# Optimization experiments

Measured on AMD Instinct MI355X. Metric: run time of the kernel, lower is better.

Reference implementation:

```python
import jax, jax.numpy as jnp
import numpy as np
from jax import lax

MAX_SCALE = 4
SCALES = [2 ** i for i in range(1, MAX_SCALE + 1)]  # [2, 4, 8, 16]
EPS = 1e-6
BN_EPS = 1e-3  # keras BatchNormalization default epsilon


def _box_sum(x, r):
    # DepthwiseConv2D with ones kernel, SAME zero padding == box sum window
    return lax.reduce_window(x, 0.0, lax.add, (1, r, r, 1), (1, 1, 1, 1), 'SAME')


def setup_inputs() -> dict:
    key = jax.random.key(0)
    k1, k2 = jax.random.split(key)
    B, H, W, C, K = 4, 224, 224, 64, 8
    return {
        'x': jax.random.normal(k1, (B, H, W, C), dtype=jnp.float32),
        'ols_weights': jnp.ones((MAX_SCALE,), jnp.float32),
        'anchors': jax.random.normal(k2, (C, K), dtype=jnp.float32),
        'hist_widths': jnp.ones((C, K), jnp.float32),
        'bn_gamma': jnp.ones((C,), jnp.float32),
        'bn_beta': jnp.zeros((C,), jnp.float32),
        'bn_mean': jnp.zeros((C,), jnp.float32),
        'bn_var': jnp.ones((C,), jnp.float32),
    }


def reference(x, ols_weights, anchors, hist_widths, bn_gamma, bn_beta, bn_mean, bn_var):
    # --- sample min-max scaling to [0, 1] per sample ---
    xmin = jnp.min(x, axis=(1, 2, 3), keepdims=True)
    xmax = jnp.max(x, axis=(1, 2, 3), keepdims=True)
    xs = (x - xmin) / (xmax - xmin + EPS)

    # --- multi-scale box measures: [B,H,W,C,S] ---
    measures = jnp.stack([_box_sum(xs, r) for r in SCALES], axis=-1)

    # --- weighted OLS slope of log(measure) vs log(scale) -> local alpha ---
    ly = jnp.log(measures + EPS)                         # [B,H,W,C,S]
    lr = jnp.log(jnp.asarray(SCALES, jnp.float32))       # [S]
    w = ols_weights                                       # [S]
    wsum = jnp.sum(w)
    lr_bar = jnp.sum(w * lr) / wsum
    ly_bar = jnp.sum(w * ly, axis=-1, keepdims=True) / wsum
    dx = lr - lr_bar                                      # [S]
    num = jnp.sum(w * dx * (ly - ly_bar), axis=-1)        # [B,H,W,C]
    den = jnp.sum(w * dx * dx)
    alphas = num / den

    # --- batch norm (inference mode, training=False) ---
    a = bn_gamma * (alphas - bn_mean) * lax.rsqrt(bn_var + BN_EPS) + bn_beta

    # --- triangular soft histogram over k anchors, relu'd and summed ---
    hist = 1.0 - hist_widths * jnp.abs(a[..., None] - anchors)  # [B,H,W,C,K]
    soft_counts = jnp.sum(jax.nn.relu(hist), axis=-1)           # [B,H,W,C]

    return x + jax.nn.sigmoid(soft_counts)
```

## Files before the change

### kernel.cpp

```cpp
#include <hip/hip_runtime.h>
#include <math.h>

#define B 4
#define H 224
#define W 224
#define C 64
#define K 8
#define WC (W*C)
#define HWC (H*W*C)

__device__ inline float wave_reduce_min(float v) {
  #pragma unroll
  for (int off = 32; off > 0; off >>= 1)
    v = fminf(v, __shfl_down(v, off, 64));
  return v;
}
__device__ inline float wave_reduce_max(float v) {
  #pragma unroll
  for (int off = 32; off > 0; off >>= 1)
    v = fmaxf(v, __shfl_down(v, off, 64));
  return v;
}

__global__ __launch_bounds__(256) void k_minmax_part(const float* __restrict__ x,
                                                     float* __restrict__ scratch) {
  int s   = blockIdx.x >> 9;
  int blk = blockIdx.x & 511;
  const float4* xs = (const float4*)(x + (size_t)s * HWC);
  const int n4 = HWC / 4;
  float vmin = INFINITY, vmax = -INFINITY;
  for (int i = blk*256 + threadIdx.x; i < n4; i += 512*256) {
    float4 v = xs[i];
    vmin = fminf(vmin, fminf(fminf(v.x, v.y), fminf(v.z, v.w)));
    vmax = fmaxf(vmax, fmaxf(fmaxf(v.x, v.y), fmaxf(v.z, v.w)));
  }
  __shared__ float smin[4], smax[4];
  float wmin = wave_reduce_min(vmin), wmax = wave_reduce_max(vmax);
  int wave = threadIdx.x >> 6, lane = threadIdx.x & 63;
  if (lane == 0) { smin[wave] = wmin; smax[wave] = wmax; }
  __syncthreads();
  if (threadIdx.x == 0) {
    float m = fminf(fminf(smin[0], smin[1]), fminf(smin[2], smin[3]));
    float M = fmaxf(fmaxf(smax[0], smax[1]), fmaxf(smax[2], smax[3]));
    scratch[blockIdx.x]        = m;
    scratch[2048 + blockIdx.x] = M;
  }
}

__global__ __launch_bounds__(256) void k_vpfx4(const float* __restrict__ x,
                                               const float* __restrict__ scratch,
                                               float* __restrict__ P) {
  int bid = blockIdx.x;
  int b = bid / W, w = bid % W;
  int seg = threadIdx.x >> 4;
  int chg = threadIdx.x & 15;
  int wv  = threadIdx.x >> 6;

  float vmn = fminf(scratch[b*512 + threadIdx.x], scratch[b*512 + 256 + threadIdx.x]);
  float vmx = fmaxf(scratch[2048 + b*512 + threadIdx.x], scratch[2048 + b*512 + 256 + threadIdx.x]);
  __shared__ float smin[4], smax[4];
  float wmn = wave_reduce_min(vmn), wmx = wave_reduce_max(vmx);
  if ((threadIdx.x & 63) == 0) { smin[wv] = wmn; smax[wv] = wmx; }
  __syncthreads();
  float xmin = fminf(fminf(smin[0], smin[1]), fminf(smin[2], smin[3]));
  float xmax = fmaxf(fmaxf(smax[0], smax[1]), fmaxf(smax[2], smax[3]));
  float inv  = 1.0f / (xmax - xmin + 1e-6f);

  const size_t colbase = (size_t)b*HWC + (size_t)w*C;
  const float4* xp4 = (const float4*)(x + colbase);
  const int RS4 = WC / 4;
  const int r0 = seg * 14;

  float4 v4[14];
  #pragma unroll
  for (int j = 0; j < 14; ++j) v4[j] = xp4[(size_t)(r0 + j) * RS4 + chg];

  float4 s4 = v4[0];
  #pragma unroll
  for (int j = 1; j < 14; ++j) {
    s4.x += v4[j].x; s4.y += v4[j].y; s4.z += v4[j].z; s4.w += v4[j].w;
  }

  __shared__ float4 segsum[16][16];
  segsum[seg][chg] = s4;
  __syncthreads();

  float4 o4 = {0.f, 0.f, 0.f, 0.f};
  #pragma unroll
  for (int ss = 0; ss < 16; ++ss) {
    if (ss < seg) {
      float4 t = segsum[ss][chg];
      o4.x += t.x; o4.y += t.y; o4.z += t.z; o4.w += t.w;
    }
  }

  float4* Pp4 = (float4*)(P + colbase);
  float ax = o4.x, ay = o4.y, az = o4.z, aw = o4.w;
  #pragma unroll
  for (int j = 0; j < 14; ++j) {
    ax += v4[j].x; ay += v4[j].y; az += v4[j].z; aw += v4[j].w;
    float sub = (float)(r0 + j + 1) * xmin;
    float4 outv;
    outv.x = (ax - sub) * inv;
    outv.y = (ay - sub) * inv;
    outv.z = (az - sub) * inv;
    outv.w = (aw - sub) * inv;
    Pp4[(size_t)(r0 + j) * RS4 + chg] = outv;
  }
}

__global__ __launch_bounds__(128) void k_main(
    const float* __restrict__ P, const float* __restrict__ x,
    const float* __restrict__ ols, const float* __restrict__ anchors,
    const float* __restrict__ hwidths, const float* __restrict__ bn_gamma,
    const float* __restrict__ bn_beta, const float* __restrict__ bn_mean,
    const float* __restrict__ bn_var, float* __restrict__ out) {
  int xcd  = blockIdx.x & 7;
  int i    = blockIdx.x >> 3;
  int rg   = xcd * 112 + (i >> 2);
  int wave = threadIdx.x >> 6, c = threadIdx.x & 63;
  int chunk = (i & 3) * 2 + wave;
  int b = rg / H, h = rg % H;
  int w0 = chunk * 28;

  const float LN2 = 0.69314718055994530942f;
  float wg0 = ols[0], wg1 = ols[1], wg2 = ols[2], wg3 = ols[3];
  float l0 = LN2, l1 = 2.f*LN2, l2 = 3.f*LN2, l3 = 4.f*LN2;
  float wsum = wg0 + wg1 + wg2 + wg3;
  float lrbar = (wg0*l0 + wg1*l1 + wg2*l2 + wg3*l3) / wsum;
  float d0 = l0-lrbar, d1 = l1-lrbar, d2 = l2-lrbar, d3 = l3-lrbar;
  float den = wg0*d0*d0 + wg1*d1*d1 + wg2*d2*d2 + wg3*d3*d3;
  float c0 = wg0*d0/den, c1 = wg1*d1/den, c2 = wg2*d2/den, c3 = wg3*d3/den;

  float scl  = bn_gamma[c] * rsqrtf(bn_var[c] + 1e-3f);
  float bofs = bn_beta[c] - bn_mean[c] * scl;
  float anc[K], wd[K];
  #pragma unroll
  for (int k = 0; k < K; ++k) { anc[k] = anchors[c*K + k]; wd[k] = hwidths[c*K + k]; }

  const int hiA[4] = {1, 2, 4, 8};
  const int loA[4] = {0, 1, 3, 7};
  const float* pt[4]; const float* pb[4]; float fb[4];
  #pragma unroll
  for (int s = 0; s < 4; ++s) {
    int ht = h + hiA[s]; if (ht > H-1) ht = H-1;
    int hb = h - loA[s] - 1;
    int hbc = hb < 0 ? 0 : hb;
    pt[s] = P + (size_t)b*HWC + (size_t)ht*WC + c;
    pb[s] = P + (size_t)b*HWC + (size_t)hbc*WC + c;
    fb[s] = hb < 0 ? 0.f : 1.f;
  }

  const float* xrow = x   + (size_t)b*HWC + (size_t)h*WC + c;
  float*       orow = out + (size_t)b*HWC + (size_t)h*WC + c;

  float ring2[2]   = {0,0};
  float ring4[4]   = {0,0,0,0};
  float ring8[8]   = {0,0,0,0,0,0,0,0};
  float ring16[16] = {0,0,0,0,0,0,0,0,0,0,0,0,0,0,0,0};
  float T0 = 0.f, T1 = 0.f, T2 = 0.f, T3 = 0.f;
  float abuf[8] = {0,0,0,0,0,0,0,0};

  for (int t0 = 0; t0 < 48; t0 += 16) {
    #pragma unroll
    for (int u = 0; u < 16; ++u) {
      int t  = t0 + u;
      int wr = w0 - 7 + t;
      float m0 = 0.f, m1 = 0.f, m2 = 0.f, m3 = 0.f;
      if (wr >= 0 && wr < W) {
        int off = wr * C;
        m0 = pt[0][off] - fb[0]*pb[0][off];
        m1 = pt[1][off] - fb[1]*pb[1][off];
        m2 = pt[2][off] - fb[2]*pb[2][off];
        m3 = pt[3][off] - fb[3]*pb[3][off];
      }
      T0 += m0 - ring2[u&1];  ring2[u&1]  = m0;
      T1 += m1 - ring4[u&3];  ring4[u&3]  = m1;
      T2 += m2 - ring8[u&7];  ring8[u&7]  = m2;
      T3 += m3 - ring16[u];   ring16[u]   = m3;
      abuf[(u+7)&7] += c0 * __logf(fmaxf(T0, 0.f) + 1e-6f);
      abuf[(u+6)&7] += c1 * __logf(fmaxf(T1, 0.f) + 1e-6f);
      abuf[(u+4)&7] += c2 * __logf(fmaxf(T2, 0.f) + 1e-6f);
      abuf[u&7]     += c3 * __logf(fmaxf(T3, 0.f) + 1e-6f);
      int ig = w0 - 15 + t;
      if (t >= 15 && ig <= w0 + 27) {
        float alpha = abuf[u&7];
        float a = alpha * scl + bofs;
        float sc = 0.f;
        #pragma unroll
        for (int k = 0; k < K; ++k)
          sc += fmaxf(0.f, 1.f - wd[k]*fabsf(a - anc[k]));
        float sig = 1.f / (1.f + __expf(-sc));
        float xv = __builtin_nontemporal_load(&xrow[ig*C]);
        __builtin_nontemporal_store(xv + sig, &orow[ig*C]);
      }
      abuf[u&7] = 0.f;
    }
  }
}


extern "C" void kernel_launch(void* const* d_in, const int* in_sizes, int n_in,
                              void* d_out, int out_size, void* d_ws, size_t ws_size,
                              hipStream_t stream) {
  const float* x        = (const float*)d_in[0];
  const float* ols      = (const float*)d_in[1];
  const float* anchors  = (const float*)d_in[2];
  const float* hwidths  = (const float*)d_in[3];
  const float* bn_gamma = (const float*)d_in[4];
  const float* bn_beta  = (const float*)d_in[5];
  const float* bn_mean  = (const float*)d_in[6];
  const float* bn_var   = (const float*)d_in[7];
  float* out = (float*)d_out;
  float* P   = (float*)d_ws;
  float* scratch = out;

  hipLaunchKernelGGL(k_minmax_part, dim3(2048),  dim3(256), 0, stream, x, scratch);
  hipLaunchKernelGGL(k_vpfx4,       dim3(B*W),   dim3(256), 0, stream, x, scratch, P);
  hipLaunchKernelGGL(k_main,        dim3(B*H*4), dim3(128), 0, stream,
                     P, x, ols, anchors, hwidths, bn_gamma, bn_beta, bn_mean, bn_var, out);
}
```

Before: 214.1 us.

## Fuse vertical prefix pass into main kernel with direct 16-row box sums

Removes the column prefix-sum kernel and its intermediate P buffer. The fused kernel reads 16 input rows directly per column and builds the vertical box sums for all scales, then applies the horizontal sliding windows. Min-max normalisation is folded algebraically into offsets (Anh, Kin, epsp) instead of being applied to every element. Each block now covers a whole row, with two waves processing an edge segment and an interior segment interleaved. This saves a full write and read of a tensor-sized intermediate plus one launch, at the cost of about 16x redundant reads of x that must be served from cache, and higher register pressure.

Result: faster. 190.5 us (-11.0%).

```diff
diff --git a/kernel.cpp b/kernel.cpp
--- a/kernel.cpp
+++ b/kernel.cpp
@@ -21,6 +21,7 @@
     v = fmaxf(v, __shfl_down(v, off, 64));
   return v;
 }
+
 
 __global__ __launch_bounds__(256) void k_minmax_part(const float* __restrict__ x,
                                                      float* __restrict__ scratch) {
@@ -46,6 +47,181 @@
     scratch[2048 + blockIdx.x] = M;
   }
 }
+
+__global__ __launch_bounds__(128) void k_fused2(
+    const float* __restrict__ x, const float* __restrict__ scratch,
+    const float* __restrict__ ols, const float* __restrict__ anchors,
+    const float* __restrict__ hwidths, const float* __restrict__ bn_gamma,
+    const float* __restrict__ bn_beta, const float* __restrict__ bn_mean,
+    const float* __restrict__ bn_var, float* __restrict__ out) {
+  int xcd  = blockIdx.x & 7;
+  int i    = blockIdx.x >> 3;
+  int rg   = xcd * 112 + i;
+  int wave = threadIdx.x >> 6, c = threadIdx.x & 63;
+  int b = rg / H, h = rg % H;
+  const int wE0 = wave ? 168 : 0;
+  const int wI0 = wave ? 112 : 56;
+
+  float vmn = fminf(fminf(scratch[b*512 + threadIdx.x],
+                          scratch[b*512 + threadIdx.x + 128]),
+                    fminf(scratch[b*512 + threadIdx.x + 256],
+                          scratch[b*512 + threadIdx.x + 384]));
+  float vmx = fmaxf(fmaxf(scratch[2048 + b*512 + threadIdx.x],
+                          scratch[2048 + b*512 + threadIdx.x + 128]),
+                    fmaxf(scratch[2048 + b*512 + threadIdx.x + 256],
+                          scratch[2048 + b*512 + threadIdx.x + 384]));
+  vmn = wave_reduce_min(vmn);
+  vmx = wave_reduce_max(vmx);
+  __shared__ float sred[4];
+  if ((threadIdx.x & 63) == 0) { sred[wave*2] = vmn; sred[wave*2+1] = vmx; }
+  __syncthreads();
+  float xmin = fminf(sred[0], sred[2]);
+  float xmax = fmaxf(sred[1], sred[3]);
+  float rng  = xmax - xmin + 1e-6f;
+  float epsp = 1e-6f * rng;
+
+  const float LN2 = 0.69314718055994530942f;
+  float wg0 = ols[0], wg1 = ols[1], wg2 = ols[2], wg3 = ols[3];
+  float l0 = LN2, l1 = 2.f*LN2, l2 = 3.f*LN2, l3 = 4.f*LN2;
+  float wsum = wg0 + wg1 + wg2 + wg3;
+  float lrbar = (wg0*l0 + wg1*l1 + wg2*l2 + wg3*l3) / wsum;
+  float d0 = l0-lrbar, d1 = l1-lrbar, d2 = l2-lrbar, d3 = l3-lrbar;
+  float den = wg0*d0*d0 + wg1*d1*d1 + wg2*d2*d2 + wg3*d3*d3;
+  float c0 = wg0*d0/den, c1 = wg1*d1/den, c2 = wg2*d2/den, c3 = wg3*d3/den;
+
+  float scl  = bn_gamma[c] * rsqrtf(bn_var[c] + 1e-3f);
+  float bofs = bn_beta[c] - bn_mean[c] * scl;
+  float anc[K], wd[K];
+  #pragma unroll
+  for (int k = 0; k < K; ++k) { anc[k] = anchors[c*K + k]; wd[k] = hwidths[c*K + k]; }
+
+  const int hiA[4] = {1, 2, 4, 8};
+  const int loA[4] = {0, 1, 3, 7};
+  const int rA[4]  = {2, 4, 8, 16};
+  float Anh[4], Kin[4];
+  #pragma unroll
+  for (int s = 0; s < 4; ++s) {
+    int ht = h + hiA[s]; if (ht > H-1) ht = H-1;
+    int h0 = h - loA[s]; if (h0 < 0) h0 = 0;
+    int nv = ht - h0 + 1;
+    Anh[s] = -(float)nv * xmin;
+    Kin[s] = (float)rA[s] * Anh[s] + epsp;
+  }
+
+  const float* rb[16]; float fr[16];
+  const size_t sbase = (size_t)b * HWC;
+  #pragma unroll
+  for (int r16 = 0; r16 < 16; ++r16) {
+    int r  = h - 7 + r16;
+    int rc = r < 0 ? 0 : (r > H-1 ? H-1 : r);
+    rb[r16] = x + sbase + (size_t)rc * WC;
+    fr[r16] = (r >= 0 && r <= H-1) ? 1.f : 0.f;
+  }
+
+  float* orow = out + sbase + (size_t)h*WC + c;
+
+  float rE2[2]={0,0}, rE4[4]={0,0,0,0}, rE8[8]={0,0,0,0,0,0,0,0};
+  float rE16[16]={0,0,0,0,0,0,0,0,0,0,0,0,0,0,0,0};
+  float rI2[2]={0,0}, rI4[4]={0,0,0,0}, rI8[8]={0,0,0,0,0,0,0,0};
+  float rI16[16]={0,0,0,0,0,0,0,0,0,0,0,0,0,0,0,0};
+  float xrE[8]={0,0,0,0,0,0,0,0}, xrI[8]={0,0,0,0,0,0,0,0};
+  float TE0=0.f,TE1=0.f,TE2=0.f,TE3=0.f, TI0=0.f,TI1=0.f,TI2=0.f,TI3=0.f;
+  float abE[8]={0,0,0,0,0,0,0,0}, abI[8]={0,0,0,0,0,0,0,0};
+
+#define FSTEP(u_, t_) do {                                                    \
+    int t = (t_);                                                             \
+                                                 \
+    int wrE = wE0 - 7 + t;                                                    \
+    float mE0, mE1, mE2, mE3, xEnew;                                          \
+    mE0 = mE1 = mE2 = mE3 = 0.f; xEnew = 0.f;                                 \
+    if (wrE >= 0 && wrE < W) {                                                \
+      int off = wrE * C + c;                                                  \
+      float v00=rb[0][off],  v01=rb[1][off],  v02=rb[2][off],  v03=rb[3][off];\
+      float v04=rb[4][off],  v05=rb[5][off],  v06=rb[6][off],  v07=rb[7][off];\
+      float v08=rb[8][off],  v09=rb[9][off],  v10=rb[10][off], v11=rb[11][off];\
+      float v12=rb[12][off], v13=rb[13][off], v14=rb[14][off], v15=rb[15][off];\
+      mE0 = fr[7]*v07 + fr[8]*v08;                                            \
+      mE1 = mE0 + fr[6]*v06 + fr[9]*v09;                                      \
+      mE2 = mE1 + fr[4]*v04 + fr[5]*v05 + fr[10]*v10 + fr[11]*v11;            \
+      mE3 = mE2 + fr[0]*v00 + fr[1]*v01 + fr[2]*v02 + fr[3]*v03               \
+                + fr[12]*v12 + fr[13]*v13 + fr[14]*v14 + fr[15]*v15;          \
+      xEnew = v07;                                                            \
+    }                                                                         \
+                              \
+    int wrI = wI0 - 7 + t;                                                    \
+    int offI = wrI * C + c;                                                   \
+    float w00=rb[0][offI],  w01=rb[1][offI],  w02=rb[2][offI],  w03=rb[3][offI];\
+    float w04=rb[4][offI],  w05=rb[5][offI],  w06=rb[6][offI],  w07=rb[7][offI];\
+    float w08=rb[8][offI],  w09=rb[9][offI],  w10=rb[10][offI], w11=rb[11][offI];\
+    float w12=rb[12][offI], w13=rb[13][offI], w14=rb[14][offI], w15=rb[15][offI];\
+    float mI0 = fr[7]*w07 + fr[8]*w08;                                        \
+    float mI1 = mI0 + fr[6]*w06 + fr[9]*w09;                                  \
+    float mI2 = mI1 + fr[4]*w04 + fr[5]*w05 + fr[10]*w10 + fr[11]*w11;        \
+    float mI3 = mI2 + fr[0]*w00 + fr[1]*w01 + fr[2]*w02 + fr[3]*w03           \
+              + fr[12]*w12 + fr[13]*w13 + fr[14]*w14 + fr[15]*w15;            \
+    float xInew = w07;                                                        \
+    float xEold = xrE[(u_)&7]; xrE[(u_)&7] = xEnew;                           \
+    float xIold = xrI[(u_)&7]; xrI[(u_)&7] = xInew;                           \
+    TE0 += mE0 - rE2[(u_)&1];   rE2[(u_)&1]   = mE0;                          \
+    TE1 += mE1 - rE4[(u_)&3];   rE4[(u_)&3]   = mE1;                          \
+    TE2 += mE2 - rE8[(u_)&7];   rE8[(u_)&7]   = mE2;                          \
+    TE3 += mE3 - rE16[(u_)&15]; rE16[(u_)&15] = mE3;                          \
+    TI0 += mI0 - rI2[(u_)&1];   rI2[(u_)&1]   = mI0;                          \
+    TI1 += mI1 - rI4[(u_)&3];   rI4[(u_)&3]   = mI1;                          \
+    TI2 += mI2 - rI8[(u_)&7];   rI8[(u_)&7]   = mI2;                          \
+    TI3 += mI3 - rI16[(u_)&15]; rI16[(u_)&15] = mI3;                          \
+          \
+         \
+    float nh0 = (float)(min(wrE, W-1) - max(wrE-1,  0) + 1);                  \
+    float nh1 = (float)(min(wrE, W-1) - max(wrE-3,  0) + 1);                  \
+    float nh2 = (float)(min(wrE, W-1) - max(wrE-7,  0) + 1);                  \
+    float nh3 = (float)(min(wrE, W-1) - max(wrE-15, 0) + 1);                  \
+    float aE0 = fmaxf(fmaf(Anh[0], nh0, TE0) + epsp, epsp);                   \
+    float aE1 = fmaxf(fmaf(Anh[1], nh1, TE1) + epsp, epsp);                   \
+    float aE2 = fmaxf(fmaf(Anh[2], nh2, TE2) + epsp, epsp);                   \
+    float aE3 = fmaxf(fmaf(Anh[3], nh3, TE3) + epsp, epsp);                   \
+    float aI0 = fmaxf(TI0 + Kin[0], epsp);                                    \
+    float aI1 = fmaxf(TI1 + Kin[1], epsp);                                    \
+    float aI2 = fmaxf(TI2 + Kin[2], epsp);                                    \
+    float aI3 = fmaxf(TI3 + Kin[3], epsp);                                    \
+    abE[((u_)+7)&7] += c0 * __logf(aE0);                                      \
+    abE[((u_)+6)&7] += c1 * __logf(aE1);                                      \
+    abE[((u_)+4)&7] += c2 * __logf(aE2);                                      \
+    abE[(u_)&7]     += c3 * __logf(aE3);                                      \
+    abI[((u_)+7)&7] += c0 * __logf(aI0);                                      \
+    abI[((u_)+6)&7] += c1 * __logf(aI1);                                      \
+    abI[((u_)+4)&7] += c2 * __logf(aI2);                                      \
+    abI[(u_)&7]     += c3 * __logf(aI3);                                      \
+    if (t >= 15) {                                                            \
+      int igE = wE0 - 15 + t;                                                 \
+      float aa = abE[(u_)&7] * scl + bofs;                                    \
+      float sc = 0.f;                                                         \
+      _Pragma("unroll")                                                       \
+      for (int k = 0; k < K; ++k)                                             \
+        sc += fmaxf(0.f, 1.f - wd[k]*fabsf(aa - anc[k]));                     \
+      float sig = 1.f / (1.f + __expf(-sc));                                  \
+      __builtin_nontemporal_store(xEold + sig, &orow[igE*C]);                 \
+      int igI = wI0 - 15 + t;                                                 \
+      float ab = abI[(u_)&7] * scl + bofs;                                    \
+      float sc2 = 0.f;                                                        \
+      _Pragma("unroll")                                                       \
+      for (int k = 0; k < K; ++k)                                             \
+        sc2 += fmaxf(0.f, 1.f - wd[k]*fabsf(ab - anc[k]));                    \
+      float sig2 = 1.f / (1.f + __expf(-sc2));                                \
+      __builtin_nontemporal_store(xIold + sig2, &orow[igI*C]);                \
+    }                                                                         \
+    abE[(u_)&7] = 0.f; abI[(u_)&7] = 0.f;                                     \
+  } while (0)
+
+  for (int t0 = 0; t0 < 64; t0 += 16) {
+    #pragma unroll
+    for (int u = 0; u < 16; ++u) FSTEP(u, t0 + u);
+  }
+  #pragma unroll
+  for (int u = 0; u < 7; ++u) FSTEP(u, 64 + u);
+#undef FSTEP
+}
+
 
 __global__ __launch_bounds__(256) void k_vpfx4(const float* __restrict__ x,
                                                const float* __restrict__ scratch,
@@ -212,11 +388,20 @@
   const float* bn_mean  = (const float*)d_in[6];
   const float* bn_var   = (const float*)d_in[7];
   float* out = (float*)d_out;
-  float* P   = (float*)d_ws;
-  float* scratch = out;
-
-  hipLaunchKernelGGL(k_minmax_part, dim3(2048),  dim3(256), 0, stream, x, scratch);
-  hipLaunchKernelGGL(k_vpfx4,       dim3(B*W),   dim3(256), 0, stream, x, scratch, P);
-  hipLaunchKernelGGL(k_main,        dim3(B*H*4), dim3(128), 0, stream,
-                     P, x, ols, anchors, hwidths, bn_gamma, bn_beta, bn_mean, bn_var, out);
-}
+
+  if (ws_size >= 16384) {
+    float* scratch = (float*)d_ws;
+    hipLaunchKernelGGL(k_minmax_part, dim3(2048), dim3(256), 0, stream, x, scratch);
+    hipLaunchKernelGGL(k_fused2,      dim3(B*H),  dim3(128), 0, stream,
+                       x, scratch, ols, anchors, hwidths,
+                       bn_gamma, bn_beta, bn_mean, bn_var, out);
+  } else {
+    float* P = (float*)d_ws;
+    float* scratch = out;
+    hipLaunchKernelGGL(k_minmax_part, dim3(2048),  dim3(256), 0, stream, x, scratch);
+    hipLaunchKernelGGL(k_vpfx4,       dim3(B*W),   dim3(256), 0, stream, x, scratch, P);
+    hipLaunchKernelGGL(k_main,        dim3(B*H*4), dim3(128), 0, stream,
+                       P, x, ols, anchors, hwidths,
+                       bn_gamma, bn_beta, bn_mean, bn_var, out);
+  }
+}
```
